# Kernel tuning notes

Hardware: AMD Instinct MI355X
Metric: run time of the kernel (lower is better)

## Reference

```python
import jax, jax.numpy as jnp
import numpy as np

INPUT_DIM = 1024
HIDDEN_DIM = 64   # per-head dim
NUM_HEADS = 16
PROJ = HIDDEN_DIM * NUM_HEADS  # 1024


def setup_inputs() -> dict:
    key = jax.random.key(0)
    ks = jax.random.split(key, 9)
    s = 1.0 / np.sqrt(INPUT_DIM)
    x = jax.random.normal(ks[0], (4, 2048, INPUT_DIM), dtype=jnp.float32)
    # Linear weights stored [in, out] (math-equivalent to torch's W.T)
    Wq = jax.random.uniform(ks[1], (INPUT_DIM, PROJ), jnp.float32, -s, s)
    bq = jax.random.uniform(ks[2], (PROJ,), jnp.float32, -s, s)
    Wk = jax.random.uniform(ks[3], (INPUT_DIM, PROJ), jnp.float32, -s, s)
    bk = jax.random.uniform(ks[4], (PROJ,), jnp.float32, -s, s)
    Wv = jax.random.uniform(ks[5], (INPUT_DIM, PROJ), jnp.float32, -s, s)
    bv = jax.random.uniform(ks[6], (PROJ,), jnp.float32, -s, s)
    sf = 1.0 / np.sqrt(PROJ)
    Wf = jax.random.uniform(ks[7], (PROJ, HIDDEN_DIM), jnp.float32, -sf, sf)
    bf = jax.random.uniform(ks[8], (HIDDEN_DIM,), jnp.float32, -sf, sf)
    return {"x": x, "Wq": Wq, "bq": bq, "Wk": Wk, "bk": bk,
            "Wv": Wv, "bv": bv, "Wf": Wf, "bf": bf}


def reference(x, Wq, bq, Wk, bk, Wv, bv, Wf, bf):
    B, S, _ = x.shape
    def split_heads(t):  # [B,S,H*D] -> [B,H,S,D]
        return t.reshape(B, S, NUM_HEADS, HIDDEN_DIM).transpose(0, 2, 1, 3)
    q = split_heads(x @ Wq + bq)
    k = split_heads(x @ Wk + bk)
    v = split_heads(x @ Wv + bv)
    scale = 1.0 / jnp.sqrt(jnp.float32(HIDDEN_DIM))
    scores = jnp.einsum('bhqd,bhkd->bhqk', q, k) * scale  # [B,H,S,S]
    weights = jax.nn.softmax(scores, axis=-1)
    ctx = jnp.einsum('bhqk,bhkd->bhqd', weights, v)
    ctx = ctx.transpose(0, 2, 1, 3).reshape(B, S, PROJ)
    return ctx @ Wf + bf  # [B,S,HIDDEN_DIM]
```

## Files before the change

### kernel.cpp

```cpp
#include <hip/hip_runtime.h>
#include <math.h>

#define S_LEN 2048
#define NH 16
#define HD 64
#define DMODEL 1024
#define BATCH 4
#define M_TOT (BATCH * S_LEN)

typedef __attribute__((ext_vector_type(8))) short bf16x8;
typedef __attribute__((ext_vector_type(4))) float f32x4;

#define CK 0.18033688f

__device__ __forceinline__ unsigned short f2bf_rne(float f) {
    unsigned u = __float_as_uint(f);
    u += 0x7fffu + ((u >> 16) & 1u);
    return (unsigned short)(u >> 16);
}

__device__ __forceinline__ void gld16(unsigned short* lds, const unsigned short* g) {
    __builtin_amdgcn_global_load_lds(
        (const __attribute__((address_space(1))) void*)g,
        (__attribute__((address_space(3))) void*)lds, 16, 0, 0);
}

__global__ __launch_bounds__(256) void cvt_fused(
    const float* __restrict__ x,
    const float* __restrict__ Wq, const float* __restrict__ Wk,
    const float* __restrict__ Wv, const float* __restrict__ Wf,
    unsigned short* __restrict__ xb, unsigned short* __restrict__ WT)
{
    const int z = blockIdx.z;
    const int tid = threadIdx.x;

    if (z < 4) {
        if (z == 3 && blockIdx.x > 0) return;
        const float* W = (z == 0) ? Wq : (z == 1) ? Wk : (z == 2) ? Wv : Wf;
        const int ncol = (z == 3) ? 64 : DMODEL;
        unsigned short* out = WT + (size_t)z * DMODEL * DMODEL;

        __shared__ float Lt[64][65];
        const int r0 = blockIdx.y * 64;
        const int c0 = blockIdx.x * 64;

        #pragma unroll
        for (int p = 0; p < 4; p++) {
            int row = (tid >> 4) + p * 16;
            int c4 = (tid & 15) * 4;
            float4 v = *(const float4*)(W + (size_t)(r0 + row) * ncol + c0 + c4);
            Lt[row][c4 + 0] = v.x; Lt[row][c4 + 1] = v.y;
            Lt[row][c4 + 2] = v.z; Lt[row][c4 + 3] = v.w;
        }
        __syncthreads();
        #pragma unroll
        for (int p = 0; p < 4; p++) {
            int nr = (tid >> 4) + p * 16;
            int kc = (tid & 15) * 4;
            unsigned short t[4];
            #pragma unroll
            for (int j = 0; j < 4; j++) t[j] = f2bf_rne(Lt[kc + j][nr]);
            *(uint2*)(out + (size_t)(c0 + nr) * DMODEL + r0 + kc) = *(uint2*)t;
        }
    } else {
        const int gtid = (blockIdx.y * 16 + blockIdx.x) * 256 + tid;
        #pragma unroll
        for (int it = 0; it < 8; it++) {
            #pragma unroll
            for (int k = 0; k < 4; k++) {
                size_t i = ((size_t)((it * 4 + k) * 65536) + gtid) * 4;
                float4 v = *(const float4*)(x + i);
                unsigned short t[4];
                t[0] = f2bf_rne(v.x); t[1] = f2bf_rne(v.y);
                t[2] = f2bf_rne(v.z); t[3] = f2bf_rne(v.w);
                *(uint2*)(xb + i) = *(uint2*)t;
            }
        }
    }
}

__global__ __launch_bounds__(512) void qkv_fused_mfma(
    const unsigned short* __restrict__ xb,
    const unsigned short* __restrict__ WT,
    const float* __restrict__ bq, const float* __restrict__ bk,
    const float* __restrict__ bv,
    unsigned short* __restrict__ Qb, unsigned short* __restrict__ Kb,
    unsigned short* __restrict__ Vtb)
{
    __shared__ __align__(16) unsigned short Ws[24 * 512];
    __shared__ __align__(16) unsigned short Bs[32 * 512];

    const int lin = blockIdx.x;
    const int xcd = lin & 7;
    const int s   = lin >> 3;
    const int rb  = xcd * 4 + (s & 3);
    const int ocb = s >> 2;

    const int tid = threadIdx.x;
    const int lane = tid & 63, w = tid >> 6;
    const int quad = lane >> 4, l15 = lane & 15;

    const int R0  = rb * 256;
    const int OC0 = ocb * 64;

    const unsigned short* gW0 = WT +
        (size_t)(OC0 + (w >> 1) * 16 + l15) * DMODEL + (w & 1) * 32 + quad * 8;
    const unsigned short* gW1 = gW0 + (size_t)DMODEL * DMODEL;
    const unsigned short* gW2 = gW1 + (size_t)DMODEL * DMODEL;
    const unsigned short* gB0 = xb + (size_t)(R0 + w * 16 + l15) * DMODEL + quad * 8;
    const unsigned short* gB1 = gB0 + (size_t)128 * DMODEL;

    f32x4 acc[3][4][2];
    #pragma unroll
    for (int z = 0; z < 3; z++)
        #pragma unroll
        for (int i = 0; i < 4; i++)
            #pragma unroll
            for (int j = 0; j < 2; j++)
                #pragma unroll
                for (int c = 0; c < 4; c++) acc[z][i][j][c] = 0.f;

#define QKV_STAGE(K)  do {                                             \
        gld16(Ws + (0 * 8 + w) * 512, gW0 + (K));                      \
        gld16(Ws + (1 * 8 + w) * 512, gW1 + (K));                      \
        gld16(Ws + (2 * 8 + w) * 512, gW2 + (K));                      \
        gld16(Bs + ((w + 0) * 2 + 0) * 512, gB0 + (K));                \
        gld16(Bs + ((w + 0) * 2 + 1) * 512, gB0 + (K) + 32);           \
        gld16(Bs + ((w + 8) * 2 + 0) * 512, gB1 + (K));                \
        gld16(Bs + ((w + 8) * 2 + 1) * 512, gB1 + (K) + 32);           \
    } while (0)

    for (int t = 0; t < 16; ++t) {
        __syncthreads();
        QKV_STAGE(t * 64);
        __syncthreads();

        #pragma unroll
        for (int sl = 0; sl < 2; sl++) {
            bf16x8 bfr[2];
            #pragma unroll
            for (int j = 0; j < 2; j++)
                bfr[j] = *(const bf16x8*)&Bs[((2 * w + j) * 2 + sl) * 512 + lane * 8];
            #pragma unroll
            for (int z = 0; z < 3; z++) {
                bf16x8 af[4];
                #pragma unroll
                for (int i = 0; i < 4; i++)
                    af[i] = *(const bf16x8*)&Ws[(z * 8 + i * 2 + sl) * 512 + lane * 8];
                if (z != 2) {
                    #pragma unroll
                    for (int i = 0; i < 4; i++)
                        #pragma unroll
                        for (int j = 0; j < 2; j++)
                            acc[z][i][j] = __builtin_amdgcn_mfma_f32_16x16x32_bf16(
                                af[i], bfr[j], acc[z][i][j], 0, 0, 0);
                } else {
                    #pragma unroll
                    for (int i = 0; i < 4; i++)
                        #pragma unroll
                        for (int j = 0; j < 2; j++)
                            acc[2][i][j] = __builtin_amdgcn_mfma_f32_16x16x32_bf16(
                                bfr[j], af[i], acc[2][i][j], 0, 0, 0);
                }
            }
        }
    }
#undef QKV_STAGE

    #pragma unroll
    for (int z = 0; z < 2; z++) {
        unsigned short* out = (z == 0) ? Qb : Kb;
        const float* bias = (z == 0) ? bq : bk;
        const float qs = (z == 0) ? CK : 1.0f;
        #pragma unroll
        for (int i = 0; i < 4; i++) {
            int oc = OC0 + i * 16 + quad * 4;
            float4 bv4 = *(const float4*)&bias[oc];
            #pragma unroll
            for (int j = 0; j < 2; j++) {
                int row = R0 + w * 32 + j * 16 + l15;
                unsigned short t4[4];
                t4[0] = f2bf_rne((acc[z][i][j][0] + bv4.x) * qs);
                t4[1] = f2bf_rne((acc[z][i][j][1] + bv4.y) * qs);
                t4[2] = f2bf_rne((acc[z][i][j][2] + bv4.z) * qs);
                t4[3] = f2bf_rne((acc[z][i][j][3] + bv4.w) * qs);
                *(uint2*)(out + (size_t)row * DMODEL + oc) = *(uint2*)t4;
            }
        }
    }
    {
        const int b = R0 >> 11;
        const int sbase = (R0 & 2047) + w * 32;
        #pragma unroll
        for (int i = 0; i < 4; i++) {
            int oc = OC0 + i * 16 + l15;
            float bvv = bv[oc];
            #pragma unroll
            for (int j = 0; j < 2; j++) {
                int sq = sbase + j * 16 + quad * 4;
                unsigned short t4[4];
                t4[0] = f2bf_rne(acc[2][i][j][0] + bvv);
                t4[1] = f2bf_rne(acc[2][i][j][1] + bvv);
                t4[2] = f2bf_rne(acc[2][i][j][2] + bvv);
                t4[3] = f2bf_rne(acc[2][i][j][3] + bvv);
                *(uint2*)(Vtb + (size_t)(b * DMODEL + oc) * S_LEN + sq) = *(uint2*)t4;
            }
        }
    }
}

__global__ __launch_bounds__(512, 4) void flash_attn_mfma(
    const unsigned short* __restrict__ Qg,
    const unsigned short* __restrict__ Kg,
    const unsigned short* __restrict__ Vtg,
    unsigned short* __restrict__ ctxb)
{
    __shared__ __align__(16) unsigned short Ks[16 * 512];
    __shared__ __align__(16) unsigned short Vs[16 * 512];
    __shared__ __align__(16) unsigned short Ps[16 * 512];

    const int tid  = threadIdx.x;
    const int lane = tid & 63, w = tid >> 6;
    const int quad = lane >> 4, l15 = lane & 15;

    const int lin = blockIdx.x;
    const int xcd = lin & 7;
    const int s   = lin >> 3;
    const int bh  = xcd + 8 * (s >> 3);
    const int qblk = s & 7;
    const int b = bh >> 4, h = bh & 15;
    const int r0 = qblk * 256;

    bf16x8 qf[2][2];
    #pragma unroll
    for (int nt = 0; nt < 2; nt++)
        #pragma unroll
        for (int ds = 0; ds < 2; ds++)
            qf[nt][ds] = *(const bf16x8*)(Qg +
                (size_t)(b * S_LEN + r0 + w * 32 + nt * 16 + l15) * DMODEL +
                h * HD + ds * 32 + quad * 8);

    const int sw = w & 3;
    const unsigned short* gK = Kg +
        (size_t)(b * S_LEN + sw * 32 + l15) * DMODEL + h * HD + quad * 8;
    const unsigned short* gV = Vtg +
        ((size_t)(bh * HD + sw * 16 + l15)) * S_LEN + quad * 8;

    f32x4 O[2][4], lsum[2];
    #pragma unroll
    for (int rt = 0; rt < 2; rt++) {
        #pragma unroll
        for (int c = 0; c < 4; c++) lsum[rt][c] = 0.f;
        #pragma unroll
        for (int dt = 0; dt < 4; dt++)
            #pragma unroll
            for (int c = 0; c < 4; c++) O[rt][dt][c] = 0.f;
    }

    f32x4 zero4;
    #pragma unroll
    for (int c = 0; c < 4; c++) zero4[c] = 0.f;
    bf16x8 ones;
    #pragma unroll
    for (int c = 0; c < 8; c++) ones[c] = (short)0x3F80;

    for (int st = 0; st < S_LEN / 128; st++) {
        __syncthreads();
        if (w < 4) {
            gld16(Ks + (w * 4 + 0) * 512, gK);
            gld16(Ks + (w * 4 + 1) * 512, gK + 32);
            gld16(Ks + (w * 4 + 2) * 512, gK + (size_t)16 * DMODEL);
            gld16(Ks + (w * 4 + 3) * 512, gK + (size_t)16 * DMODEL + 32);
            gK += (size_t)128 * DMODEL;
        } else {
            gld16(Vs + (sw * 4 + 0) * 512, gV);
            gld16(Vs + (sw * 4 + 1) * 512, gV + 32);
            gld16(Vs + (sw * 4 + 2) * 512, gV + 64);
            gld16(Vs + (sw * 4 + 3) * 512, gV + 96);
            gV += 128;
        }
        __syncthreads();

        #pragma unroll
        for (int r = 0; r < 4; r++) {
            f32x4 sc[2][2];
            {
                bf16x8 kf0 = *(const bf16x8*)&Ks[((r * 2 + 0) * 2 + 0) * 512 + lane * 8];
                bf16x8 kf1 = *(const bf16x8*)&Ks[((r * 2 + 1) * 2 + 0) * 512 + lane * 8];
                sc[0][0] = __builtin_amdgcn_mfma_f32_16x16x32_bf16(kf0, qf[0][0], zero4, 0, 0, 0);
                sc[0][1] = __builtin_amdgcn_mfma_f32_16x16x32_bf16(kf0, qf[1][0], zero4, 0, 0, 0);
                sc[1][0] = __builtin_amdgcn_mfma_f32_16x16x32_bf16(kf1, qf[0][0], zero4, 0, 0, 0);
                sc[1][1] = __builtin_amdgcn_mfma_f32_16x16x32_bf16(kf1, qf[1][0], zero4, 0, 0, 0);
                kf0 = *(const bf16x8*)&Ks[((r * 2 + 0) * 2 + 1) * 512 + lane * 8];
                kf1 = *(const bf16x8*)&Ks[((r * 2 + 1) * 2 + 1) * 512 + lane * 8];
                sc[0][0] = __builtin_amdgcn_mfma_f32_16x16x32_bf16(kf0, qf[0][1], sc[0][0], 0, 0, 0);
                sc[0][1] = __builtin_amdgcn_mfma_f32_16x16x32_bf16(kf0, qf[1][1], sc[0][1], 0, 0, 0);
                sc[1][0] = __builtin_amdgcn_mfma_f32_16x16x32_bf16(kf1, qf[0][1], sc[1][0], 0, 0, 0);
                sc[1][1] = __builtin_amdgcn_mfma_f32_16x16x32_bf16(kf1, qf[1][1], sc[1][1], 0, 0, 0);
            }

            #pragma unroll
            for (int nt = 0; nt < 2; nt++) {
                #pragma unroll
                for (int mt = 0; mt < 2; mt++) {
                    unsigned u[4];
                    #pragma unroll
                    for (int c = 0; c < 4; c++)
                        u[c] = __float_as_uint(__builtin_amdgcn_exp2f(sc[mt][nt][c]));
                    uint2 pk;
                    pk.x = __builtin_amdgcn_perm(u[1], u[0], 0x07060302u);
                    pk.y = __builtin_amdgcn_perm(u[3], u[2], 0x07060302u);
                    int off = (w * 2 + nt) * 512 + (mt * 2 + (quad >> 1)) * 128 +
                              l15 * 8 + (quad & 1) * 4;
                    *(uint2*)&Ps[off] = pk;
                }
            }

            bf16x8 pf0 = *(const bf16x8*)&Ps[(w * 2 + 0) * 512 + lane * 8];
            bf16x8 pf1 = *(const bf16x8*)&Ps[(w * 2 + 1) * 512 + lane * 8];
            lsum[0] = __builtin_amdgcn_mfma_f32_16x16x32_bf16(pf0, ones, lsum[0], 0, 0, 0);
            lsum[1] = __builtin_amdgcn_mfma_f32_16x16x32_bf16(pf1, ones, lsum[1], 0, 0, 0);
            #pragma unroll
            for (int dt = 0; dt < 4; dt++) {
                bf16x8 vf = *(const bf16x8*)&Vs[(dt * 4 + r) * 512 + lane * 8];
                O[0][dt] = __builtin_amdgcn_mfma_f32_16x16x32_bf16(pf0, vf, O[0][dt], 0, 0, 0);
                O[1][dt] = __builtin_amdgcn_mfma_f32_16x16x32_bf16(pf1, vf, O[1][dt], 0, 0, 0);
            }
        }
    }

    const size_t srow = (size_t)(b * S_LEN + r0 + w * 32);
    #pragma unroll
    for (int rt = 0; rt < 2; rt++) {
        #pragma unroll
        for (int reg = 0; reg < 4; reg++) {
            float li = 1.0f / lsum[rt][reg];
            size_t rowoff = (srow + rt * 16 + quad * 4 + reg) * DMODEL + h * HD + l15;
            #pragma unroll
            for (int dt = 0; dt < 4; dt++)
                ctxb[rowoff + dt * 16] = f2bf_rne(O[rt][dt][reg] * li);
        }
    }
}

__global__ __launch_bounds__(512) void out_proj_mfma(
    const unsigned short* __restrict__ ctxb,
    const unsigned short* __restrict__ WfT,
    const float* __restrict__ bfb,
    float* __restrict__ out)
{
    __shared__ float Red[8 * 1024];

    const int tid = threadIdx.x;
    const int lane = tid & 63, w = tid >> 6;
    const int quad = lane >> 4, l15 = lane & 15;
    const int m0 = blockIdx.x * 16;

    const unsigned short* pA = ctxb + (size_t)(m0 + l15) * DMODEL + w * 128 + quad * 8;
    const unsigned short* pB = WfT + (size_t)l15 * DMODEL + w * 128 + quad * 8;

    f32x4 acc[4];
    #pragma unroll
    for (int j = 0; j < 4; j++)
        #pragma unroll
        for (int c = 0; c < 4; c++) acc[j][c] = 0.f;

    #pragma unroll
    for (int k0 = 0; k0 < 128; k0 += 32) {
        bf16x8 af = *(const bf16x8*)(pA + k0);
        #pragma unroll
        for (int j = 0; j < 4; j++) {
            bf16x8 bfr = *(const bf16x8*)(pB + (size_t)j * 16 * DMODEL + k0);
            acc[j] = __builtin_amdgcn_mfma_f32_16x16x32_bf16(af, bfr, acc[j], 0, 0, 0);
        }
    }

    #pragma unroll
    for (int j = 0; j < 4; j++)
        #pragma unroll
        for (int reg = 0; reg < 4; reg++)
            Red[w * 1024 + lane * 16 + j * 4 + reg] = acc[j][reg];
    __syncthreads();

    const int row = tid >> 5;
    const int c0  = (tid & 31) * 2;
    float2 o;
    float* op = &o.x;
    #pragma unroll
    for (int cc = 0; cc < 2; cc++) {
        int col = c0 + cc;
        int idx = ((row >> 2) * 16 + (col & 15)) * 16 + (col >> 4) * 4 + (row & 3);
        float s = 0.f;
        #pragma unroll
        for (int wv = 0; wv < 8; wv++) s += Red[wv * 1024 + idx];
        op[cc] = s + bfb[col];
    }
    *(float2*)(out + (size_t)(m0 + row) * HD + c0) = o;
}

extern "C" void kernel_launch(void* const* d_in, const int* in_sizes, int n_in,
                              void* d_out, int out_size, void* d_ws, size_t ws_size,
                              hipStream_t stream)
{
    (void)in_sizes; (void)n_in; (void)out_size; (void)ws_size;
    const float* x  = (const float*)d_in[0];
    const float* Wq = (const float*)d_in[1];
    const float* bq = (const float*)d_in[2];
    const float* Wk = (const float*)d_in[3];
    const float* bk = (const float*)d_in[4];
    const float* Wv = (const float*)d_in[5];
    const float* bv = (const float*)d_in[6];
    const float* Wf = (const float*)d_in[7];
    const float* bf = (const float*)d_in[8];
    float* out = (float*)d_out;

    char* wsb = (char*)d_ws;
    unsigned short* xb   = (unsigned short*)wsb;
    unsigned short* ctxb = (unsigned short*)wsb;
    unsigned short* WT   = xb + (size_t)M_TOT * DMODEL;
    unsigned short* WfT  = WT + (size_t)3 * DMODEL * DMODEL;
    unsigned short* Qb   = (unsigned short*)(wsb + (size_t)32 * 1024 * 1024);
    unsigned short* Kb   = Qb + (size_t)M_TOT * DMODEL;
    unsigned short* Vtb  = Kb + (size_t)M_TOT * DMODEL;

    cvt_fused<<<dim3(16, 16, 5), 256, 0, stream>>>(x, Wq, Wk, Wv, Wf, xb, WT);
    qkv_fused_mfma<<<dim3(512), 512, 0, stream>>>(xb, WT, bq, bk, bv, Qb, Kb, Vtb);
    flash_attn_mfma<<<dim3(512), 512, 0, stream>>>(Qb, Kb, Vtb, ctxb);
    out_proj_mfma<<<dim3(M_TOT / 16), 512, 0, stream>>>(ctxb, WfT, bf, out);
}
```

Measured before the change: 277.1 us.

## Double-buffer QKV weight tiles and load x fragments directly into registers

Rewrites the QKV projection main loop to double-buffer the weight tiles in LDS, so the next stage's global-to-LDS loads overlap the current stage's MFMAs. The x operand no longer goes through LDS; each wave loads its own fragments straight from global memory into registers, also one step ahead. This is meant to hide global load latency and remove the LDS traffic and space used for x. In exchange it uses more VGPRs for the prefetched fragments, and the per-lane direct global reads of x may be less coalesced.

```diff
diff --git a/kernel.cpp b/kernel.cpp
--- a/kernel.cpp
+++ b/kernel.cpp
@@ -87,8 +87,7 @@
     unsigned short* __restrict__ Qb, unsigned short* __restrict__ Kb,
     unsigned short* __restrict__ Vtb)
 {
-    __shared__ __align__(16) unsigned short Ws[24 * 512];
-    __shared__ __align__(16) unsigned short Bs[32 * 512];
+    __shared__ __align__(16) unsigned short Ws[2][24 * 512];
 
     const int lin = blockIdx.x;
     const int xcd = lin & 7;
@@ -107,8 +106,9 @@
         (size_t)(OC0 + (w >> 1) * 16 + l15) * DMODEL + (w & 1) * 32 + quad * 8;
     const unsigned short* gW1 = gW0 + (size_t)DMODEL * DMODEL;
     const unsigned short* gW2 = gW1 + (size_t)DMODEL * DMODEL;
-    const unsigned short* gB0 = xb + (size_t)(R0 + w * 16 + l15) * DMODEL + quad * 8;
-    const unsigned short* gB1 = gB0 + (size_t)128 * DMODEL;
+    const unsigned short* gx0 = xb +
+        (size_t)(R0 + w * 32 + l15) * DMODEL + quad * 8;
+    const unsigned short* gx1 = gx0 + (size_t)16 * DMODEL;
 
     f32x4 acc[3][4][2];
     #pragma unroll
@@ -120,52 +120,69 @@
                 #pragma unroll
                 for (int c = 0; c < 4; c++) acc[z][i][j][c] = 0.f;
 
-#define QKV_STAGE(K)  do {                                             \
-        gld16(Ws + (0 * 8 + w) * 512, gW0 + (K));                      \
-        gld16(Ws + (1 * 8 + w) * 512, gW1 + (K));                      \
-        gld16(Ws + (2 * 8 + w) * 512, gW2 + (K));                      \
-        gld16(Bs + ((w + 0) * 2 + 0) * 512, gB0 + (K));                \
-        gld16(Bs + ((w + 0) * 2 + 1) * 512, gB0 + (K) + 32);           \
-        gld16(Bs + ((w + 8) * 2 + 0) * 512, gB1 + (K));                \
-        gld16(Bs + ((w + 8) * 2 + 1) * 512, gB1 + (K) + 32);           \
+#define QKV_STAGEW(BUF, K)  do {                                       \
+        gld16(Ws[BUF] + (0 * 8 + w) * 512, gW0 + (K));                 \
+        gld16(Ws[BUF] + (1 * 8 + w) * 512, gW1 + (K));                 \
+        gld16(Ws[BUF] + (2 * 8 + w) * 512, gW2 + (K));                 \
     } while (0)
 
-    for (int t = 0; t < 16; ++t) {
+#define QKV_LOADX(XF, K)  do {                                         \
+        XF[0][0] = *(const bf16x8*)(gx0 + (K));                        \
+        XF[0][1] = *(const bf16x8*)(gx0 + (K) + 32);                   \
+        XF[1][0] = *(const bf16x8*)(gx1 + (K));                        \
+        XF[1][1] = *(const bf16x8*)(gx1 + (K) + 32);                   \
+    } while (0)
+
+#define QKV_COMPUTE(BUF, XF)  do {                                     \
+        _Pragma("unroll")                                              \
+        for (int sl = 0; sl < 2; sl++) {                               \
+            _Pragma("unroll")                                          \
+            for (int z = 0; z < 3; z++) {                              \
+                bf16x8 af[4];                                          \
+                _Pragma("unroll")                                      \
+                for (int i = 0; i < 4; i++)                            \
+                    af[i] = *(const bf16x8*)&Ws[BUF][(z * 8 + i * 2 + sl) * 512 + lane * 8]; \
+                if (z != 2) {                                          \
+                    _Pragma("unroll")                                  \
+                    for (int i = 0; i < 4; i++)                        \
+                        _Pragma("unroll")                              \
+                        for (int j = 0; j < 2; j++)                    \
+                            acc[z][i][j] = __builtin_amdgcn_mfma_f32_16x16x32_bf16( \
+                                af[i], XF[j][sl], acc[z][i][j], 0, 0, 0); \
+                } else {                                               \
+                    _Pragma("unroll")                                  \
+                    for (int i = 0; i < 4; i++)                        \
+                        _Pragma("unroll")                              \
+                        for (int j = 0; j < 2; j++)                    \
+                            acc[2][i][j] = __builtin_amdgcn_mfma_f32_16x16x32_bf16( \
+                                XF[j][sl], af[i], acc[2][i][j], 0, 0, 0); \
+                }                                                      \
+            }                                                          \
+        }                                                              \
+    } while (0)
+
+    bf16x8 xA[2][2], xB[2][2];
+
+    QKV_STAGEW(0, 0);
+    QKV_LOADX(xA, 0);
+
+    #pragma unroll 1
+    for (int tt = 0; tt < 16; tt += 2) {
         __syncthreads();
-        QKV_STAGE(t * 64);
+        QKV_STAGEW(1, (tt + 1) * 64);
+        QKV_LOADX(xB, (tt + 1) * 64);
+        QKV_COMPUTE(0, xA);
+
         __syncthreads();
-
-        #pragma unroll
-        for (int sl = 0; sl < 2; sl++) {
-            bf16x8 bfr[2];
-            #pragma unroll
-            for (int j = 0; j < 2; j++)
-                bfr[j] = *(const bf16x8*)&Bs[((2 * w + j) * 2 + sl) * 512 + lane * 8];
-            #pragma unroll
-            for (int z = 0; z < 3; z++) {
-                bf16x8 af[4];
-                #pragma unroll
-                for (int i = 0; i < 4; i++)
-                    af[i] = *(const bf16x8*)&Ws[(z * 8 + i * 2 + sl) * 512 + lane * 8];
-                if (z != 2) {
-                    #pragma unroll
-                    for (int i = 0; i < 4; i++)
-                        #pragma unroll
-                        for (int j = 0; j < 2; j++)
-                            acc[z][i][j] = __builtin_amdgcn_mfma_f32_16x16x32_bf16(
-                                af[i], bfr[j], acc[z][i][j], 0, 0, 0);
-                } else {
-                    #pragma unroll
-                    for (int i = 0; i < 4; i++)
-                        #pragma unroll
-                        for (int j = 0; j < 2; j++)
-                            acc[2][i][j] = __builtin_amdgcn_mfma_f32_16x16x32_bf16(
-                                bfr[j], af[i], acc[2][i][j], 0, 0, 0);
-                }
-            }
-        }
-    }
-#undef QKV_STAGE
+        if (tt < 14) {
+            QKV_STAGEW(0, (tt + 2) * 64);
+            QKV_LOADX(xA, (tt + 2) * 64);
+        }
+        QKV_COMPUTE(1, xB);
+    }
+#undef QKV_STAGEW
+#undef QKV_LOADX
+#undef QKV_COMPUTE
 
     #pragma unroll
     for (int z = 0; z < 2; z++) {
```

Result: faster. 256.9 us (-7.3%).
